# Performance work log

Measured on AMD Instinct MI355X. Metric: run time of the kernel, lower is better.

Reference implementation:

```python
import jax, jax.numpy as jnp
import numpy as np

B, S, E, H, D = 4, 2048, 1024, 16, 64   # batch, seq, embed, heads, head_dim
NUM_BUCKETS, MAX_DISTANCE = 32, 128


def _relative_position_bucket(relative_position, num_buckets, max_distance):
    # causal T5-style bucketing
    max_exact = num_buckets // 2
    max_distance = max(max_distance, max_exact + 1)
    distance = jnp.maximum(-relative_position, 0)
    is_small = distance < max_exact
    safe_distance = jnp.maximum(distance, 1)
    log_scale = jnp.log(safe_distance / max_exact) / jnp.log(max_distance / max_exact)
    large_bucket = max_exact + (log_scale * (num_buckets - max_exact)).astype(jnp.int32)
    large_bucket = jnp.minimum(large_bucket, num_buckets - 1)
    return jnp.where(is_small, distance, large_bucket)


def setup_inputs() -> dict:
    key = jax.random.key(0)
    ks = jax.random.split(key, 7)
    w_scale = 1.0 / np.sqrt(E)
    inputs_q = jax.random.normal(ks[0], (B, S, E), jnp.float32)
    inputs_kv = jax.random.normal(ks[1], (B, S, E), jnp.float32)
    Wq = jax.random.normal(ks[2], (E, H * D), jnp.float32) * w_scale
    Wk = jax.random.normal(ks[3], (E, H * D), jnp.float32) * w_scale
    Wv = jax.random.normal(ks[4], (E, H * D), jnp.float32) * w_scale
    Wo = jax.random.normal(ks[5], (H * D, E), jnp.float32) * (1.0 / np.sqrt(H * D))
    rel_bias = jax.random.normal(ks[6], (H, NUM_BUCKETS), jnp.float32) * 0.02
    mask = jnp.tril(jnp.ones((S, S), dtype=bool))[None, None]  # [1,1,Q,K] causal
    return {"inputs_q": inputs_q, "inputs_kv": inputs_kv, "mask": mask,
            "Wq": Wq, "Wk": Wk, "Wv": Wv, "Wo": Wo, "rel_bias": rel_bias}


def reference(inputs_q, inputs_kv, mask, Wq, Wk, Wv, Wo, rel_bias):
    batch, q_len, embed = inputs_q.shape
    k_len = inputs_kv.shape[1]
    q = (inputs_q @ Wq).reshape(batch, q_len, H, D)
    k = (inputs_kv @ Wk).reshape(batch, k_len, H, D)
    v = (inputs_kv @ Wv).reshape(batch, k_len, H, D)
    attention = jnp.einsum("bqhd,bkhd->bhqk", q, k) * (1.0 / jnp.sqrt(D))
    # T5 relative position bias
    rel_pos = jnp.arange(k_len, dtype=jnp.int32)[None, :] - jnp.arange(q_len, dtype=jnp.int32)[:, None]
    bucket = _relative_position_bucket(rel_pos, NUM_BUCKETS, MAX_DISTANCE)  # [Q,K]
    attention = attention + jnp.take(rel_bias, bucket, axis=1)[None]  # [1,H,Q,K]
    attention = jnp.where(mask, attention, jnp.finfo(jnp.float32).min)
    normalized = jax.nn.softmax(attention, axis=-1)
    output = jnp.einsum("bhqk,bkhd->bqhd", normalized, v).reshape(batch, q_len, H * D)
    return output @ Wo
```

## Files before the change

### kernel.cpp

```cpp
#include <hip/hip_runtime.h>

typedef unsigned short u16;
typedef unsigned int u32;
typedef __bf16 bf16x8 __attribute__((ext_vector_type(8)));
typedef float f32x2 __attribute__((ext_vector_type(2)));
typedef float f32x4 __attribute__((ext_vector_type(4)));
typedef float f32x16 __attribute__((ext_vector_type(16)));

#define S_LEN 2048
#define EMB 1024
#define NH 16
#define HD 64
#define LOG2E 1.44269504088896f
#define QSCALE (0.125f * LOG2E)
#define THRL 11.5415603f
#define FB(r) ((((r) ^ ((r) >> 2))) & 3)
#define MEMB asm volatile("" ::: "memory")

__device__ __forceinline__ u16 f2bf(float f) {
  union { float f; unsigned u; } v; v.f = f;
  unsigned r = (v.u + 0x7fffu + ((v.u >> 16) & 1u)) >> 16;
  return (u16)r;
}

__device__ __forceinline__ u32 packbf(float a, float b) {
  union { __bf16 h[2]; u32 u; } x;
  x.h[0] = (__bf16)a; x.h[1] = (__bf16)b;
  return x.u;
}

__device__ __forceinline__ void g2l16(const void* g, void* l) {
  __builtin_amdgcn_global_load_lds(
      (const unsigned int __attribute__((address_space(1)))*)g,
      (unsigned int __attribute__((address_space(3)))*)l, 16, 0, 0);
}

__device__ __forceinline__ float permswap_max(float a) {
  auto r = __builtin_amdgcn_permlane32_swap(__float_as_int(a), __float_as_int(a), false, false);
  return fmaxf(__int_as_float(r[0]), __int_as_float(r[1]));
}
__device__ __forceinline__ float permswap_add(float a) {
  auto r = __builtin_amdgcn_permlane32_swap(__float_as_int(a), __float_as_int(a), false, false);
  return __int_as_float(r[0]) + __int_as_float(r[1]);
}

__device__ __forceinline__ void phase_end() {
  asm volatile("s_waitcnt lgkmcnt(0)" ::: "memory");
  asm volatile("s_waitcnt vmcnt(0)" ::: "memory");
  __builtin_amdgcn_s_barrier();
  MEMB;
}


__global__ void cvt_bf16_2(const float* __restrict__ aq, const float* __restrict__ akv,
                           u16* __restrict__ dq, u16* __restrict__ dkv) {
  int i = blockIdx.x * blockDim.x + threadIdx.x;
  const float4* s;
  ushort4* d;
  int j;
  if (i < 2097152) {
    s = (const float4*)aq; d = (ushort4*)dq; j = i;
  } else {
    s = (const float4*)akv; d = (ushort4*)dkv; j = i - 2097152;
  }
  float4 f = s[j];
  ushort4 o;
  o.x = f2bf(f.x); o.y = f2bf(f.y); o.z = f2bf(f.z); o.w = f2bf(f.w);
  d[j] = o;
}

__global__ void transcvt4(const float* __restrict__ W0, const float* __restrict__ W1,
                          const float* __restrict__ W2, const float* __restrict__ W3,
                          u16* __restrict__ Dqkv, u16* __restrict__ Do) {
  __shared__ float t[32][33];
  const int z = blockIdx.z;
  const float* W = (z == 0) ? W0 : (z == 1) ? W1 : (z == 2) ? W2 : W3;
  u16* Wt = (z < 3) ? (Dqkv + (size_t)z * 1048576) : Do;
  int k0 = blockIdx.x * 32, n0 = blockIdx.y * 32;
  int tx = threadIdx.x & 31, ty = threadIdx.x >> 5;
#pragma unroll
  for (int i = 0; i < 4; i++) t[ty + i * 8][tx] = W[(k0 + ty + i * 8) * 1024 + n0 + tx];
  __syncthreads();
#pragma unroll
  for (int i = 0; i < 4; i++) Wt[(n0 + ty + i * 8) * 1024 + k0 + tx] = f2bf(t[tx][ty + i * 8]);
}

__global__ void build_bias(const float* __restrict__ rel, float* __restrict__ tbl) {
  int i = blockIdx.x * 256 + threadIdx.x;
  int h = i >> 11, dist = i & 2047;
  int bk;
  if (dist < 16) {
    bk = dist;
  } else {
    float ls = logf((float)dist * (1.0f / 16.0f)) * (1.0f / logf(8.0f));
    bk = 16 + (int)(ls * 16.0f);
    if (bk > 31) bk = 31;
  }
  tbl[i] = rel[h * 32 + bk] * LOG2E;
}


__global__ __launch_bounds__(256, 3) void gemm_qkv(const u16* __restrict__ Aq,
                                                   const u16* __restrict__ Akv,
                                                   const u16* __restrict__ Wt,
                                                   u16* __restrict__ QKV, float qscale) {
  constexpr int K = EMB;
  __shared__ u16 As[3][128 * 32];
  __shared__ u16 Bs[3][128 * 32];

  const int bid = blockIdx.x;
  const int xcd = bid & 7, idx = bid >> 3;
  const int mt = xcd * 8 + (idx & 7);
  const int nt = idx >> 3;
  const int m0 = mt * 128;
  const int n0 = nt * 128;
  const int mat = n0 >> 10;
  const u16* A = (mat == 0) ? Aq : Akv;

  const int tid = threadIdx.x;
  const int lane = tid & 63;
  const int wid = tid >> 6;
  const int wm = (wid >> 1) * 64;
  const int wn = (wid & 1) * 64;
  const int la = lane & 15;
  const int lg = lane >> 4;

  const int r0 = tid >> 2;
  const int c0 = ((tid & 3) ^ FB(r0)) * 8;
  const u16* gA = A + (size_t)(m0 + r0) * K + c0;
  const u16* gB = Wt + (size_t)(n0 + r0) * K + c0;

  auto stage = [&](int b) {
    u16* lA = As[b] + tid * 8;
    u16* lB = Bs[b] + tid * 8;
    g2l16(gA, lA);
    g2l16(gA + 64 * K, lA + 2048);
    g2l16(gB, lB);
    g2l16(gB + 64 * K, lB + 2048);
    gA += 32;
    gB += 32;
  };

  f32x4 acc[4][4] = {};

  stage(0);
  stage(1);
  asm volatile("s_waitcnt vmcnt(4)" ::: "memory");
  __builtin_amdgcn_s_barrier();
  MEMB;

  int cur = 0;
  for (int t = 0; t < 32; ++t) {
    if (t < 30) {
      int nxt = cur + 2;
      if (nxt > 2) nxt -= 3;
      stage(nxt);
    }

    bf16x8 af[4], bb[4];
#pragma unroll
    for (int mf = 0; mf < 4; mf++) {
      int row = wm + mf * 16 + la;
      af[mf] = *(const bf16x8*)&As[cur][row * 32 + ((lg ^ FB(row)) << 3)];
    }
#pragma unroll
    for (int nf = 0; nf < 4; nf++) {
      int row = wn + nf * 16 + la;
      bb[nf] = *(const bf16x8*)&Bs[cur][row * 32 + ((lg ^ FB(row)) << 3)];
    }
    __builtin_amdgcn_s_setprio(1);
#pragma unroll
    for (int mf = 0; mf < 4; mf++)
#pragma unroll
      for (int nf = 0; nf < 4; nf++)
        acc[mf][nf] =
            __builtin_amdgcn_mfma_f32_16x16x32_bf16(bb[nf], af[mf], acc[mf][nf], 0, 0, 0);
    __builtin_amdgcn_s_setprio(0);

    asm volatile("s_waitcnt lgkmcnt(0)" ::: "memory");
    if (t < 30) asm volatile("s_waitcnt vmcnt(4)" ::: "memory");
    else        asm volatile("s_waitcnt vmcnt(0)" ::: "memory");
    __builtin_amdgcn_s_barrier();
    MEMB;

    cur = (cur == 2) ? 0 : cur + 1;
  }

  const float sc = (mat == 0) ? qscale : 1.0f;
  const size_t base = (size_t)mat << 23;
  if (mat < 2) {
#pragma unroll
    for (int mf = 0; mf < 4; mf++) {
      const int m = m0 + wm + mf * 16 + la;
      const int b = m >> 11, s = m & 2047;
#pragma unroll
      for (int nf = 0; nf < 4; nf++) {
        const int n = n0 + wn + nf * 16 + lg * 4;
        const int hh = (n >> 6) & 15, d0 = n & 63;
        ushort4 ov;
        ov.x = f2bf(acc[mf][nf][0] * sc);
        ov.y = f2bf(acc[mf][nf][1] * sc);
        ov.z = f2bf(acc[mf][nf][2] * sc);
        ov.w = f2bf(acc[mf][nf][3] * sc);
        *(ushort4*)&QKV[base + (((size_t)(b * 16 + hh) * 2048 + s) << 6) + d0] = ov;
      }
    }
  } else {
#pragma unroll
    for (int mf = 0; mf < 4; mf++) {
      const int m = m0 + wm + mf * 16 + la;
      const int b = m >> 11, s = m & 2047;
#pragma unroll
      for (int nf = 0; nf < 4; nf++)
#pragma unroll
        for (int r = 0; r < 4; r++) {
          const int n = n0 + wn + nf * 16 + lg * 4 + r;
          const int hh = (n >> 6) & 15, d = n & 63;
          QKV[base + (((size_t)(b * 16 + hh) * 64 + d) << 11) + s] = f2bf(acc[mf][nf][r]);
        }
    }
  }
}


__global__ __launch_bounds__(256, 3) void gemm_out(const u16* __restrict__ A,
                                                   const u16* __restrict__ Bt,
                                                   float* __restrict__ C) {
  constexpr int K = EMB;
  __shared__ u16 As[3][128 * 32];
  __shared__ u16 Bs[3][128 * 32];
  const int bid = blockIdx.x;
  const int xcd = bid & 7, idx = bid >> 3;
  const int mt = xcd * 8 + (idx & 7);
  const int nt = idx >> 3;
  const int m0 = mt * 128;
  const int n0 = nt * 128;
  const int tid = threadIdx.x;
  const int lane = tid & 63;
  const int wid = tid >> 6;
  const int wm = (wid >> 1) * 64;
  const int wn = (wid & 1) * 64;
  const int la = lane & 15;
  const int lg = lane >> 4;

  const int r0 = tid >> 2;
  const int c0 = ((tid & 3) ^ FB(r0)) * 8;
  const u16* gA = A + (size_t)(m0 + r0) * K + c0;
  const u16* gB = Bt + (size_t)(n0 + r0) * K + c0;

  auto stage = [&](int b) {
    u16* lA = As[b] + tid * 8;
    u16* lB = Bs[b] + tid * 8;
    g2l16(gA, lA);
    g2l16(gA + 64 * K, lA + 2048);
    g2l16(gB, lB);
    g2l16(gB + 64 * K, lB + 2048);
    gA += 32;
    gB += 32;
  };

  f32x4 acc[4][4] = {};

  stage(0);
  stage(1);
  asm volatile("s_waitcnt vmcnt(4)" ::: "memory");
  __builtin_amdgcn_s_barrier();
  MEMB;

  int cur = 0;
  for (int t = 0; t < 32; ++t) {
    if (t < 30) {
      int nxt = cur + 2;
      if (nxt > 2) nxt -= 3;
      stage(nxt);
    }

    bf16x8 af[4], bb[4];
#pragma unroll
    for (int mf = 0; mf < 4; mf++) {
      int row = wm + mf * 16 + la;
      af[mf] = *(const bf16x8*)&As[cur][row * 32 + ((lg ^ FB(row)) << 3)];
    }
#pragma unroll
    for (int nf = 0; nf < 4; nf++) {
      int row = wn + nf * 16 + la;
      bb[nf] = *(const bf16x8*)&Bs[cur][row * 32 + ((lg ^ FB(row)) << 3)];
    }
    __builtin_amdgcn_s_setprio(1);
#pragma unroll
    for (int mf = 0; mf < 4; mf++)
#pragma unroll
      for (int nf = 0; nf < 4; nf++)
        acc[mf][nf] =
            __builtin_amdgcn_mfma_f32_16x16x32_bf16(bb[nf], af[mf], acc[mf][nf], 0, 0, 0);
    __builtin_amdgcn_s_setprio(0);

    asm volatile("s_waitcnt lgkmcnt(0)" ::: "memory");
    if (t < 30) asm volatile("s_waitcnt vmcnt(4)" ::: "memory");
    else        asm volatile("s_waitcnt vmcnt(0)" ::: "memory");
    __builtin_amdgcn_s_barrier();
    MEMB;

    cur = (cur == 2) ? 0 : cur + 1;
  }

#pragma unroll
  for (int mf = 0; mf < 4; mf++) {
    const int m = m0 + wm + mf * 16 + la;
#pragma unroll
    for (int nf = 0; nf < 4; nf++) {
      const int n = n0 + wn + nf * 16 + lg * 4;
      float4 ov;
      ov.x = acc[mf][nf][0];
      ov.y = acc[mf][nf][1];
      ov.z = acc[mf][nf][2];
      ov.w = acc[mf][nf][3];
      *(float4*)&C[(size_t)m * 1024 + n] = ov;
    }
  }
}


__device__ __forceinline__ void softmax_repack(const f32x16* sacc, int kv0, int qw, int q, int hi,
                                               const float* bias_s, float bias31, float& mrun,
                                               float& lrun, f32x16& o0, f32x16& o1,
                                               u32 (&paw)[4][4]) {
  f32x2 pf[16];
  float adde = 0.f;
  if (kv0 + 176 <= qw) {
#pragma unroll
    for (int j = 0; j < 16; j++) {
      const int nf = j >> 3, r = (j & 7) * 2;
      pf[j] = (f32x2){sacc[nf][r], sacc[nf][r + 1]};
    }
    adde = bias31;
  } else {
    const int qb2 = q - kv0 - 4 * hi;
    const float* bp = bias_s + (qb2 - 59);
    if (kv0 + 63 <= qw) {
#pragma unroll
      for (int j = 0; j < 16; j++) {
        const int nf = j >> 3, r = (j & 7) * 2;
        const int Cn = nf * 32 + (r & 3) + ((r >> 2) << 3);
        f32x2 bv = {bp[59 - Cn], bp[58 - Cn]};
        pf[j] = (f32x2){sacc[nf][r], sacc[nf][r + 1]} + bv;
      }
    } else {
#pragma unroll
      for (int j = 0; j < 16; j++) {
        const int nf = j >> 3, r = (j & 7) * 2;
        const int Cn = nf * 32 + (r & 3) + ((r >> 2) << 3);
        pf[j].x = (Cn <= qb2) ? (sacc[nf][r] + bp[59 - Cn]) : -1e30f;
        pf[j].y = (Cn + 1 <= qb2) ? (sacc[nf][r + 1] + bp[58 - Cn]) : -1e30f;
      }
    }
  }

  f32x2 t8[8];
#pragma unroll
  for (int i = 0; i < 8; i++) t8[i] = __builtin_elementwise_max(pf[i], pf[i + 8]);
#pragma unroll
  for (int i = 0; i < 4; i++) t8[i] = __builtin_elementwise_max(t8[i], t8[i + 4]);
  f32x2 m2 = __builtin_elementwise_max(__builtin_elementwise_max(t8[0], t8[1]),
                                       __builtin_elementwise_max(t8[2], t8[3]));
  float mt = fmaxf(m2.x, m2.y) + adde;
  mt = permswap_max(mt);

  if (__any(mt > mrun + THRL)) {
    float mn = fmaxf(mrun, mt);
    float s = exp2f(mrun - mn);
    mrun = mn;
    lrun *= s;
    o0 *= s;
    o1 *= s;
  }
  const f32x2 ec2 = {adde - mrun, adde - mrun};

  f32x2 s8[8];
#pragma unroll
  for (int j = 0; j < 16; j++) {
    f32x2 a = pf[j] + ec2;
    f32x2 p = {exp2f(a.x), exp2f(a.y)};
    pf[j] = p;
    if (j < 8) s8[j] = p;
    else s8[j - 8] += p;
  }
#pragma unroll
  for (int i = 0; i < 4; i++) s8[i] += s8[i + 4];
  f32x2 s2 = (s8[0] + s8[1]) + (s8[2] + s8[3]);
  lrun += permswap_add(s2.x + s2.y);

#pragma unroll
  for (int ks = 0; ks < 4; ks++) {
    const int j0b = (ks >> 1) * 8 + (ks & 1) * 4;
#pragma unroll
    for (int half = 0; half < 2; half++) {
      u32 Y0 = packbf(pf[j0b + half].x, pf[j0b + half].y);
      u32 Y1 = packbf(pf[j0b + 2 + half].x, pf[j0b + 2 + half].y);
      auto r = __builtin_amdgcn_permlane32_swap((int)Y0, (int)Y1, false, false);
      paw[ks][half] = (u32)r[0];
      paw[ks][2 + half] = (u32)r[1];
    }
  }
}

template <int CUR>
__device__ __forceinline__ void tile_body(int t, int ntblk, int qmax, int qw, int q, int hi,
                                          int la, int tid, const u16*& kp, const u16*& vp,
                                          u16 (*Ks)[64 * 64], u16 (*Vs)[64 * 64],
                                          const bf16x8 (&qfrag)[4], const float* bias_s,
                                          float bias31, float& mrun, float& lrun, f32x16& o0,
                                          f32x16& o1) {
  if (t + 1 < ntblk) {
    u16* lK = Ks[CUR ^ 1] + tid * 8;
    u16* lV = Vs[CUR ^ 1] + tid * 8;
    g2l16(kp, lK);
    g2l16(kp + 32 * 64, lK + 2048);
    g2l16(vp, lV);
    g2l16(vp + 32 * S_LEN, lV + 2048);
    kp += 4096;
    vp += 64;
  }

  const int kv0 = t << 6;
  if (kv0 <= qmax) {
    f32x16 sacc[2] = {};
    __builtin_amdgcn_s_setprio(1);
#pragma unroll
    for (int kk = 0; kk < 4; kk++)
#pragma unroll
      for (int nf = 0; nf < 2; nf++) {
        int row = nf * 32 + la;
        bf16x8 kf = *(const bf16x8*)&Ks[CUR][row * 64 + (((kk * 2 + hi) ^ (row & 7)) << 3)];
        sacc[nf] = __builtin_amdgcn_mfma_f32_32x32x16_bf16(kf, qfrag[kk], sacc[nf], 0, 0, 0);
      }
    __builtin_amdgcn_s_setprio(0);

    u32 paw[4][4];
    softmax_repack(sacc, kv0, qw, q, hi, bias_s, bias31, mrun, lrun, o0, o1, paw);

    __builtin_amdgcn_s_setprio(1);
#pragma unroll
    for (int d2 = 0; d2 < 2; d2++) {
      f32x16& oa = d2 ? o1 : o0;
#pragma unroll
      for (int ks = 0; ks < 4; ks++) {
        int row = d2 * 32 + la;
        bf16x8 vf = *(const bf16x8*)&Vs[CUR][row * 64 + (((ks * 2 + hi) ^ (row & 7)) << 3)];
        union { u32 w[4]; bf16x8 v; } pu;
        pu.w[0] = paw[ks][0]; pu.w[1] = paw[ks][1];
        pu.w[2] = paw[ks][2]; pu.w[3] = paw[ks][3];
        oa = __builtin_amdgcn_mfma_f32_32x32x16_bf16(vf, pu.v, oa, 0, 0, 0);
      }
    }
    __builtin_amdgcn_s_setprio(0);
  }

  phase_end();
}

__global__ __launch_bounds__(256, 3) void attn_kernel(const u16* __restrict__ Qb,
                                                      const u16* __restrict__ Kb,
                                                      const u16* __restrict__ Vtb,
                                                      const float* __restrict__ btbl,
                                                      u16* __restrict__ O) {
  __shared__ u16 Ks[2][64 * 64];
  __shared__ u16 Vs[2][64 * 64];
  __shared__ float bias_s[S_LEN];

  const int bh = blockIdx.x;
  const int h = bh & (NH - 1);
  const int b = bh >> 4;
  const int qt = 15 - blockIdx.y;
  const int q0 = qt * 128;
  const int tid = threadIdx.x;
  const int lane = tid & 63;
  const int w = tid >> 6;
  const int la = lane & 31;
  const int hi = lane >> 5;

  {
    const float4* src = (const float4*)(btbl + h * S_LEN);
    float4* dst = (float4*)bias_s;
    dst[tid] = src[tid];
    dst[tid + 256] = src[tid + 256];
  }

  const u16* Qg = Qb + (size_t)bh * S_LEN * HD;
  const u16* Kg = Kb + (size_t)bh * S_LEN * HD;
  const u16* Vg = Vtb + (size_t)bh * HD * S_LEN;

  const int qw = q0 + w * 32;
  const int q = qw + la;

  bf16x8 qfrag[4];
#pragma unroll
  for (int kk = 0; kk < 4; kk++)
    qfrag[kk] = *(const bf16x8*)&Qg[(size_t)q * HD + kk * 16 + hi * 8];

  f32x16 o0 = {}, o1 = {};
  float mrun = -1e30f;
  float lrun = 0.f;

  const int sr = tid >> 3;
  const int scz = ((tid & 7) ^ (sr & 7)) * 8;
  const u16* kp = Kg + sr * 64 + scz;
  const u16* vp = Vg + (size_t)sr * S_LEN + scz;

  const int ntblk = (q0 + 128) >> 6;
  const int qmax = qw + 31;

  g2l16(kp, Ks[0] + tid * 8);
  g2l16(kp + 32 * 64, Ks[0] + tid * 8 + 2048);
  g2l16(vp, Vs[0] + tid * 8);
  g2l16(vp + 32 * S_LEN, Vs[0] + tid * 8 + 2048);
  kp += 4096;
  vp += 64;
  phase_end();

  const float bias31 = bias_s[S_LEN - 1];

  int t = 0;
  while (t < ntblk) {
    tile_body<0>(t, ntblk, qmax, qw, q, hi, la, tid, kp, vp, Ks, Vs, qfrag, bias_s, bias31,
                 mrun, lrun, o0, o1);
    ++t;
    tile_body<1>(t, ntblk, qmax, qw, q, hi, la, tid, kp, vp, Ks, Vs, qfrag, bias_s, bias31,
                 mrun, lrun, o0, o1);
    ++t;
  }

  const float inv = 1.0f / lrun;
  u16* Og = O + ((size_t)(b * S_LEN + q)) * EMB + h * HD;
#pragma unroll
  for (int d2 = 0; d2 < 2; d2++) {
    const f32x16& oa = d2 ? o1 : o0;
#pragma unroll
    for (int g = 0; g < 4; g++) {
      ushort4 ov;
      ov.x = f2bf(oa[g * 4 + 0] * inv);
      ov.y = f2bf(oa[g * 4 + 1] * inv);
      ov.z = f2bf(oa[g * 4 + 2] * inv);
      ov.w = f2bf(oa[g * 4 + 3] * inv);
      *(ushort4*)&Og[d2 * 32 + g * 8 + hi * 4] = ov;
    }
  }
}


extern "C" void kernel_launch(void* const* d_in, const int* in_sizes, int n_in, void* d_out,
                              int out_size, void* d_ws, size_t ws_size, hipStream_t stream) {
  (void)in_sizes; (void)n_in; (void)out_size; (void)ws_size;
  const float* inq = (const float*)d_in[0];
  const float* inkv = (const float*)d_in[1];
  const float* Wq = (const float*)d_in[3];
  const float* Wk = (const float*)d_in[4];
  const float* Wv = (const float*)d_in[5];
  const float* Wo = (const float*)d_in[6];
  const float* rel = (const float*)d_in[7];
  float* out = (float*)d_out;

  char* ws = (char*)d_ws;
  size_t off = 0;
  auto alloc = [&](size_t bytes) {
    void* p = ws + off;
    off += (bytes + 255) & ~(size_t)255;
    return p;
  };
  u16* Aq = (u16*)alloc(16777216);
  u16* Akv = (u16*)alloc(16777216);
  u16* Wqkvt = (u16*)alloc(6291456);
  u16* Wot = (u16*)alloc(2097152);
  u16* QKV = (u16*)alloc(50331648);
  u16* Ob = (u16*)alloc(16777216);
  float* btbl = (float*)alloc(131072);

  u16* Qb = QKV;
  u16* Kb = QKV + 8388608;
  u16* Vtb = QKV + 16777216;

  cvt_bf16_2<<<16384, 256, 0, stream>>>(inq, inkv, Aq, Akv);
  transcvt4<<<dim3(32, 32, 4), 256, 0, stream>>>(Wq, Wk, Wv, Wo, Wqkvt, Wot);
  build_bias<<<128, 256, 0, stream>>>(rel, btbl);

  gemm_qkv<<<1536, 256, 0, stream>>>(Aq, Akv, Wqkvt, QKV, QSCALE);
  attn_kernel<<<dim3(64, 16), 256, 0, stream>>>(Qb, Kb, Vtb, btbl, Ob);
  gemm_out<<<512, 256, 0, stream>>>(Ob, Wot, out);
}
```

Baseline: 196.2 us.

## Software-pipeline attention: overlap next tile's QK^T with current softmax and PV

Restructures the attention loop so the QK^T MFMAs for tile t run in the same phase as the softmax and PV for tile t-1. K and V now have triple-buffered LDS with staggered prefetch and partial vmcnt waits instead of a full drain each tile. The bias table is shrunk from 2048 to 256 distances per head, relying on bias31 clamping for larger distances, which frees LDS for the extra buffers. The cost is more registers for the two score accumulators and more complex wait-count logic.

```diff
diff --git a/kernel.cpp b/kernel.cpp
--- a/kernel.cpp
+++ b/kernel.cpp
@@ -42,13 +42,6 @@
 __device__ __forceinline__ float permswap_add(float a) {
   auto r = __builtin_amdgcn_permlane32_swap(__float_as_int(a), __float_as_int(a), false, false);
   return __int_as_float(r[0]) + __int_as_float(r[1]);
-}
-
-__device__ __forceinline__ void phase_end() {
-  asm volatile("s_waitcnt lgkmcnt(0)" ::: "memory");
-  asm volatile("s_waitcnt vmcnt(0)" ::: "memory");
-  __builtin_amdgcn_s_barrier();
-  MEMB;
 }
 
 
@@ -87,7 +80,7 @@
 
 __global__ void build_bias(const float* __restrict__ rel, float* __restrict__ tbl) {
   int i = blockIdx.x * 256 + threadIdx.x;
-  int h = i >> 11, dist = i & 2047;
+  int h = i >> 8, dist = i & 255;
   int bk;
   if (dist < 16) {
     bk = dist;
@@ -404,69 +397,14 @@
   }
 }
 
-template <int CUR>
-__device__ __forceinline__ void tile_body(int t, int ntblk, int qmax, int qw, int q, int hi,
-                                          int la, int tid, const u16*& kp, const u16*& vp,
-                                          u16 (*Ks)[64 * 64], u16 (*Vs)[64 * 64],
-                                          const bf16x8 (&qfrag)[4], const float* bias_s,
-                                          float bias31, float& mrun, float& lrun, f32x16& o0,
-                                          f32x16& o1) {
-  if (t + 1 < ntblk) {
-    u16* lK = Ks[CUR ^ 1] + tid * 8;
-    u16* lV = Vs[CUR ^ 1] + tid * 8;
-    g2l16(kp, lK);
-    g2l16(kp + 32 * 64, lK + 2048);
-    g2l16(vp, lV);
-    g2l16(vp + 32 * S_LEN, lV + 2048);
-    kp += 4096;
-    vp += 64;
-  }
-
-  const int kv0 = t << 6;
-  if (kv0 <= qmax) {
-    f32x16 sacc[2] = {};
-    __builtin_amdgcn_s_setprio(1);
-#pragma unroll
-    for (int kk = 0; kk < 4; kk++)
-#pragma unroll
-      for (int nf = 0; nf < 2; nf++) {
-        int row = nf * 32 + la;
-        bf16x8 kf = *(const bf16x8*)&Ks[CUR][row * 64 + (((kk * 2 + hi) ^ (row & 7)) << 3)];
-        sacc[nf] = __builtin_amdgcn_mfma_f32_32x32x16_bf16(kf, qfrag[kk], sacc[nf], 0, 0, 0);
-      }
-    __builtin_amdgcn_s_setprio(0);
-
-    u32 paw[4][4];
-    softmax_repack(sacc, kv0, qw, q, hi, bias_s, bias31, mrun, lrun, o0, o1, paw);
-
-    __builtin_amdgcn_s_setprio(1);
-#pragma unroll
-    for (int d2 = 0; d2 < 2; d2++) {
-      f32x16& oa = d2 ? o1 : o0;
-#pragma unroll
-      for (int ks = 0; ks < 4; ks++) {
-        int row = d2 * 32 + la;
-        bf16x8 vf = *(const bf16x8*)&Vs[CUR][row * 64 + (((ks * 2 + hi) ^ (row & 7)) << 3)];
-        union { u32 w[4]; bf16x8 v; } pu;
-        pu.w[0] = paw[ks][0]; pu.w[1] = paw[ks][1];
-        pu.w[2] = paw[ks][2]; pu.w[3] = paw[ks][3];
-        oa = __builtin_amdgcn_mfma_f32_32x32x16_bf16(vf, pu.v, oa, 0, 0, 0);
-      }
-    }
-    __builtin_amdgcn_s_setprio(0);
-  }
-
-  phase_end();
-}
-
 __global__ __launch_bounds__(256, 3) void attn_kernel(const u16* __restrict__ Qb,
                                                       const u16* __restrict__ Kb,
                                                       const u16* __restrict__ Vtb,
                                                       const float* __restrict__ btbl,
                                                       u16* __restrict__ O) {
-  __shared__ u16 Ks[2][64 * 64];
-  __shared__ u16 Vs[2][64 * 64];
-  __shared__ float bias_s[S_LEN];
+  __shared__ u16 Ks[3][64 * 64];
+  __shared__ u16 Vs[3][64 * 64];
+  __shared__ float bias_s[256];
 
   const int bh = blockIdx.x;
   const int h = bh & (NH - 1);
@@ -479,12 +417,7 @@
   const int la = lane & 31;
   const int hi = lane >> 5;
 
-  {
-    const float4* src = (const float4*)(btbl + h * S_LEN);
-    float4* dst = (float4*)bias_s;
-    dst[tid] = src[tid];
-    dst[tid + 256] = src[tid + 256];
-  }
+  if (tid < 64) ((float4*)bias_s)[tid] = ((const float4*)(btbl + h * 256))[tid];
 
   const u16* Qg = Qb + (size_t)bh * S_LEN * HD;
   const u16* Kg = Kb + (size_t)bh * S_LEN * HD;
@@ -510,24 +443,111 @@
   const int ntblk = (q0 + 128) >> 6;
   const int qmax = qw + 31;
 
-  g2l16(kp, Ks[0] + tid * 8);
-  g2l16(kp + 32 * 64, Ks[0] + tid * 8 + 2048);
-  g2l16(vp, Vs[0] + tid * 8);
-  g2l16(vp + 32 * S_LEN, Vs[0] + tid * 8 + 2048);
-  kp += 4096;
-  vp += 64;
-  phase_end();
-
-  const float bias31 = bias_s[S_LEN - 1];
-
-  int t = 0;
-  while (t < ntblk) {
-    tile_body<0>(t, ntblk, qmax, qw, q, hi, la, tid, kp, vp, Ks, Vs, qfrag, bias_s, bias31,
-                 mrun, lrun, o0, o1);
-    ++t;
-    tile_body<1>(t, ntblk, qmax, qw, q, hi, la, tid, kp, vp, Ks, Vs, qfrag, bias_s, bias31,
-                 mrun, lrun, o0, o1);
-    ++t;
+  auto stK = [&](int buf, int t) {
+    u16* d = Ks[buf] + tid * 8;
+    const u16* s = kp + (size_t)t * 4096;
+    g2l16(s, d);
+    g2l16(s + 2048, d + 2048);
+  };
+  auto stV = [&](int buf, int t) {
+    u16* d = Vs[buf] + tid * 8;
+    const u16* s = vp + t * 64;
+    g2l16(s, d);
+    g2l16(s + 32 * S_LEN, d + 2048);
+  };
+  auto qk = [&](int buf, f32x16* sacc) {
+    __builtin_amdgcn_s_setprio(1);
+#pragma unroll
+    for (int kk = 0; kk < 4; kk++)
+#pragma unroll
+      for (int nf = 0; nf < 2; nf++) {
+        int row = nf * 32 + la;
+        bf16x8 kf = *(const bf16x8*)&Ks[buf][row * 64 + (((kk * 2 + hi) ^ (row & 7)) << 3)];
+        sacc[nf] = __builtin_amdgcn_mfma_f32_32x32x16_bf16(kf, qfrag[kk], sacc[nf], 0, 0, 0);
+      }
+    __builtin_amdgcn_s_setprio(0);
+  };
+  auto pv = [&](int buf, u32 (&paw)[4][4]) {
+    __builtin_amdgcn_s_setprio(1);
+#pragma unroll
+    for (int d2 = 0; d2 < 2; d2++) {
+      f32x16& oa = d2 ? o1 : o0;
+#pragma unroll
+      for (int ks = 0; ks < 4; ks++) {
+        int row = d2 * 32 + la;
+        bf16x8 vf = *(const bf16x8*)&Vs[buf][row * 64 + (((ks * 2 + hi) ^ (row & 7)) << 3)];
+        union { u32 w[4]; bf16x8 v; } pu;
+        pu.w[0] = paw[ks][0]; pu.w[1] = paw[ks][1];
+        pu.w[2] = paw[ks][2]; pu.w[3] = paw[ks][3];
+        oa = __builtin_amdgcn_mfma_f32_32x32x16_bf16(vf, pu.v, oa, 0, 0, 0);
+      }
+    }
+    __builtin_amdgcn_s_setprio(0);
+  };
+  auto endwait = [&](int t) {
+    asm volatile("s_waitcnt lgkmcnt(0)" ::: "memory");
+    if (t + 2 < ntblk)      asm volatile("s_waitcnt vmcnt(4)" ::: "memory");
+    else if (t + 1 < ntblk) asm volatile("s_waitcnt vmcnt(2)" ::: "memory");
+    else                    asm volatile("s_waitcnt vmcnt(0)" ::: "memory");
+    __builtin_amdgcn_s_barrier();
+    MEMB;
+  };
+
+  stK(0, 0);
+  stV(0, 0);
+  stK(1, 1);
+  asm volatile("s_waitcnt vmcnt(4) lgkmcnt(0)" ::: "memory");
+  __builtin_amdgcn_s_barrier();
+  MEMB;
+
+  const float bias31 = bias_s[255];
+
+  f32x16 sA[2], sB[2];
+  int kq = 1, vst = 2, kst = 0, vpv = 0;
+
+  {
+    stV(1, 1);
+    if (2 < ntblk) stK(2, 2);
+    sB[0] = (f32x16){};
+    sB[1] = (f32x16){};
+    qk(0, sB);
+    endwait(0);
+  }
+
+  auto iter_body = [&](int t, f32x16 (&swr)[2], f32x16 (&srd)[2]) {
+    if (t + 1 < ntblk) stV(vst, t + 1);
+    if (t + 2 < ntblk) stK(kst, t + 2);
+    const int kv0c = t << 6;
+    const int kv0p = kv0c - 64;
+    swr[0] = (f32x16){};
+    swr[1] = (f32x16){};
+    if (kv0c <= qmax) qk(kq, swr);
+    if (kv0p <= qmax) {
+      u32 paw[4][4];
+      softmax_repack(srd, kv0p, qw, q, hi, bias_s, bias31, mrun, lrun, o0, o1, paw);
+      pv(vpv, paw);
+    }
+    endwait(t);
+    kq = (kq == 2) ? 0 : kq + 1;
+    vst = (vst == 2) ? 0 : vst + 1;
+    kst = (kst == 2) ? 0 : kst + 1;
+    vpv = (vpv == 2) ? 0 : vpv + 1;
+  };
+
+  int t = 1;
+  for (; t + 1 < ntblk; t += 2) {
+    iter_body(t, sA, sB);
+    iter_body(t + 1, sB, sA);
+  }
+  iter_body(t, sA, sB);
+
+  {
+    const int kv0p = (ntblk - 1) << 6;
+    if (kv0p <= qmax) {
+      u32 paw[4][4];
+      softmax_repack(sA, kv0p, qw, q, hi, bias_s, bias31, mrun, lrun, o0, o1, paw);
+      pv(vpv, paw);
+    }
   }
 
   const float inv = 1.0f / lrun;
@@ -573,7 +593,7 @@
   u16* Wot = (u16*)alloc(2097152);
   u16* QKV = (u16*)alloc(50331648);
   u16* Ob = (u16*)alloc(16777216);
-  float* btbl = (float*)alloc(131072);
+  float* btbl = (float*)alloc(16384);
 
   u16* Qb = QKV;
   u16* Kb = QKV + 8388608;
@@ -581,7 +601,7 @@
 
   cvt_bf16_2<<<16384, 256, 0, stream>>>(inq, inkv, Aq, Akv);
   transcvt4<<<dim3(32, 32, 4), 256, 0, stream>>>(Wq, Wk, Wv, Wo, Wqkvt, Wot);
-  build_bias<<<128, 256, 0, stream>>>(rel, btbl);
+  build_bias<<<16, 256, 0, stream>>>(rel, btbl);
 
   gemm_qkv<<<1536, 256, 0, stream>>>(Aq, Akv, Wqkvt, QKV, QSCALE);
   attn_kernel<<<dim3(64, 16), 256, 0, stream>>>(Qb, Kb, Vtb, btbl, Ob);
```

After: 303.3 us. 1.55x slower.
